# Kernel optimization log

Measured on AMD Instinct MI355X. Metric: run time of the kernel, lower is better.

Reference implementation:

```python
import jax, jax.numpy as jnp
import numpy as np

N_SEQ, N_RES = 2048, 384
C_IN, C_OUT = 25, 64  # 23 one-hot classes + has_deletion + deletion_value


def setup_inputs() -> dict:
    key = jax.random.key(0)
    k1, k2, k3, k4, k5 = jax.random.split(key, 5)
    extra_msa = jax.random.randint(k1, (N_SEQ, N_RES), 0, 23)
    extra_has_deletion = jax.random.uniform(k2, (N_SEQ, N_RES), dtype=jnp.float32)
    extra_deletion_value = jax.random.uniform(k3, (N_SEQ, N_RES), dtype=jnp.float32)
    # torch nn.Linear convention: W is [c_out, c_in], bias [c_out]
    W = jax.random.normal(k4, (C_OUT, C_IN), dtype=jnp.float32) * (1.0 / np.sqrt(C_IN))
    b = jax.random.normal(k5, (C_OUT,), dtype=jnp.float32) * 0.02
    return {"extra_msa": extra_msa, "extra_has_deletion": extra_has_deletion,
            "extra_deletion_value": extra_deletion_value, "W": W, "b": b}


def reference(extra_msa, extra_has_deletion, extra_deletion_value, W, b):
    # [*, N_seq, N_res, 23] one-hot of residue identities
    msa_1hot = jax.nn.one_hot(extra_msa, 23, dtype=W.dtype)
    # concat with deletion features -> [*, N_seq, N_res, 25]
    msa_feat = jnp.concatenate(
        [msa_1hot, extra_has_deletion[..., None].astype(W.dtype),
         extra_deletion_value[..., None].astype(W.dtype)], axis=-1)
    # Linear: x @ W^T + b -> [*, N_seq, N_res, c_out]
    return jnp.einsum('snc,oc->sno', msa_feat, W) + b
```

## Files before the change

### kernel.cpp

```cpp
#include <hip/hip_runtime.h>
#include <hip/hip_bf16.h>


#define C_IN   25
#define C_OUT  64
#define TPAD   68
#define UNROLL 8

typedef float v4f __attribute__((ext_vector_type(4)));

__global__ __launch_bounds__(256) void extra_msa_emb_kernel(
    const int* __restrict__ msa,
    const float* __restrict__ hd,
    const float* __restrict__ dv,
    const float* __restrict__ W,
    const float* __restrict__ b,
    float* __restrict__ out) {
    const int tid   = threadIdx.x;
    const int group = tid >> 4;
    const int lane  = tid & 15;
    const int o     = lane * 4;

    const int pbase = blockIdx.x * 128 + group;

    int   cls[UNROLL];
    float h[UNROLL], d[UNROLL];
#pragma unroll
    for (int j = 0; j < UNROLL; ++j) {
        const int p = pbase + j * 16;
        cls[j] = msa[p];
        h[j]   = hd[p];
        d[j]   = dv[p];
    }

    __shared__ float T[C_IN][TPAD];
    for (int idx = tid; idx < C_IN * C_OUT; idx += 256) {
        const int c = idx >> 6;
        const int oo = idx & 63;
        float v = W[oo * C_IN + c];
        if (c < 23) v += b[oo];
        T[c][oo] = v;
    }
    __syncthreads();

    const v4f w23 = *reinterpret_cast<const v4f*>(&T[23][o]);
    const v4f w24 = *reinterpret_cast<const v4f*>(&T[24][o]);

    v4f t[UNROLL];
#pragma unroll
    for (int j = 0; j < UNROLL; ++j)
        t[j] = *reinterpret_cast<const v4f*>(&T[cls[j]][o]);

#pragma unroll
    for (int j = 0; j < UNROLL; ++j) {
        const v4f r = t[j] + h[j] * w23 + d[j] * w24;
        const long long p = (long long)(pbase + j * 16);
        __builtin_nontemporal_store(r, reinterpret_cast<v4f*>(&out[p * C_OUT + o]));
    }
}

extern "C" void kernel_launch(void* const* d_in, const int* in_sizes, int n_in,
                              void* d_out, int out_size, void* d_ws, size_t ws_size,
                              hipStream_t stream) {
    const int*   msa = (const int*)d_in[0];
    const float* hd  = (const float*)d_in[1];
    const float* dv  = (const float*)d_in[2];
    const float* W   = (const float*)d_in[3];
    const float* b   = (const float*)d_in[4];
    float* out = (float*)d_out;

    const int npos = in_sizes[0];

    const int block = 256;
    const int grid  = npos / 128;
    extra_msa_emb_kernel<<<grid, block, 0, stream>>>(msa, hd, dv, W, b, out);
}
```

Baseline: 42.01 us.

## Use persistent grid-stride blocks with software-prefetched inputs

Replaces the one-tile-per-block launch with a fixed grid of 1536 persistent blocks that loop over tiles. Each block builds the shared W+b table once, then loads the next tile's class, has-deletion and deletion-value inputs while computing and storing the current tile. The aim is to amortize the table setup over more work and hide input load latency behind output stores. In exchange it uses more registers and has fewer blocks in flight, and it assumes npos is a multiple of 128.

```diff
diff --git a/kernel.cpp b/kernel.cpp
--- a/kernel.cpp
+++ b/kernel.cpp
@@ -15,27 +15,13 @@
     const float* __restrict__ dv,
     const float* __restrict__ W,
     const float* __restrict__ b,
-    float* __restrict__ out) {
-    const int tid   = threadIdx.x;
-    const int group = tid >> 4;
-    const int lane  = tid & 15;
-    const int o     = lane * 4;
-
-    const int pbase = blockIdx.x * 128 + group;
-
-    int   cls[UNROLL];
-    float h[UNROLL], d[UNROLL];
-#pragma unroll
-    for (int j = 0; j < UNROLL; ++j) {
-        const int p = pbase + j * 16;
-        cls[j] = msa[p];
-        h[j]   = hd[p];
-        d[j]   = dv[p];
-    }
+    float* __restrict__ out,
+    int npos) {
+    const int tid = threadIdx.x;
 
     __shared__ float T[C_IN][TPAD];
     for (int idx = tid; idx < C_IN * C_OUT; idx += 256) {
-        const int c = idx >> 6;
+        const int c  = idx >> 6;
         const int oo = idx & 63;
         float v = W[oo * C_IN + c];
         if (c < 23) v += b[oo];
@@ -43,19 +29,63 @@
     }
     __syncthreads();
 
+    const int group = tid >> 4;
+    const int lane  = tid & 15;
+    const int o     = lane * 4;
+
     const v4f w23 = *reinterpret_cast<const v4f*>(&T[23][o]);
     const v4f w24 = *reinterpret_cast<const v4f*>(&T[24][o]);
 
-    v4f t[UNROLL];
+    const long long stride = (long long)gridDim.x * 128;
+    long long base = (long long)blockIdx.x * 128;
+    if (base >= npos) return;
+
+    int   cls[UNROLL];
+    float h[UNROLL], d[UNROLL];
 #pragma unroll
-    for (int j = 0; j < UNROLL; ++j)
-        t[j] = *reinterpret_cast<const v4f*>(&T[cls[j]][o]);
+    for (int j = 0; j < UNROLL; ++j) {
+        const int p = (int)base + group + j * 16;
+        cls[j] = msa[p];
+        h[j]   = hd[p];
+        d[j]   = dv[p];
+    }
+
+    for (;;) {
+        const long long nbase = base + stride;
+        const bool more = (nbase < npos);
+
+        int   ncls[UNROLL];
+        float nh[UNROLL], nd[UNROLL];
+        if (more) {
+#pragma unroll
+            for (int j = 0; j < UNROLL; ++j) {
+                const int p = (int)nbase + group + j * 16;
+                ncls[j] = msa[p];
+                nh[j]   = hd[p];
+                nd[j]   = dv[p];
+            }
+        }
+
+        v4f t[UNROLL];
+#pragma unroll
+        for (int j = 0; j < UNROLL; ++j)
+            t[j] = *reinterpret_cast<const v4f*>(&T[cls[j]][o]);
 
 #pragma unroll
-    for (int j = 0; j < UNROLL; ++j) {
-        const v4f r = t[j] + h[j] * w23 + d[j] * w24;
-        const long long p = (long long)(pbase + j * 16);
-        __builtin_nontemporal_store(r, reinterpret_cast<v4f*>(&out[p * C_OUT + o]));
+        for (int j = 0; j < UNROLL; ++j) {
+            const v4f r = t[j] + h[j] * w23 + d[j] * w24;
+            const long long p = base + group + j * 16;
+            __builtin_nontemporal_store(r, reinterpret_cast<v4f*>(&out[p * C_OUT + o]));
+        }
+
+        if (!more) break;
+        base = nbase;
+#pragma unroll
+        for (int j = 0; j < UNROLL; ++j) {
+            cls[j] = ncls[j];
+            h[j]   = nh[j];
+            d[j]   = nd[j];
+        }
     }
 }
 
@@ -72,6 +102,6 @@
     const int npos = in_sizes[0];
 
     const int block = 256;
-    const int grid  = npos / 128;
-    extra_msa_emb_kernel<<<grid, block, 0, stream>>>(msa, hd, dv, W, b, out);
+    const int grid  = 1536;
+    extra_msa_emb_kernel<<<grid, block, 0, stream>>>(msa, hd, dv, W, b, out, npos);
 }
```

Measured after the change: 37.68 us. 1.11x faster.
